# Performance work log

Hardware: AMD Instinct MI355X
Metric: run time of the kernel (lower is better)

## Reference

```python
import jax, jax.numpy as jnp
import numpy as np

N_NODES = 50000
N_EDGES = 800000
N_GRAPHS = 128
IN_F = 768
NHID = 64
HID2 = NHID * 2  # 128
N_CLS = 2


def setup_inputs() -> dict:
    key = jax.random.key(0)
    ks = jax.random.split(key, 16)
    s = lambda k, shp, fan: jax.random.normal(k, shp, jnp.float32) / np.sqrt(fan)
    return {
        "x": jax.random.normal(ks[0], (N_NODES, IN_F), jnp.float32),
        "edge_index": jax.random.randint(ks[1], (2, N_EDGES), 0, N_NODES, jnp.int64),
        "batch": jnp.sort(jax.random.randint(ks[2], (N_NODES,), 0, N_GRAPHS, jnp.int64)),
        "W1": s(ks[3], (IN_F, HID2), IN_F),
        "as1": s(ks[4], (HID2,), HID2),
        "ad1": s(ks[5], (HID2,), HID2),
        "b1": jnp.zeros((HID2,), jnp.float32),
        "W2": s(ks[6], (HID2, HID2), HID2),
        "as2": s(ks[7], (HID2,), HID2),
        "ad2": s(ks[8], (HID2,), HID2),
        "b2": jnp.zeros((HID2,), jnp.float32),
        "fc1_w": s(ks[9], (HID2, NHID), HID2),
        "fc1_b": jnp.zeros((NHID,), jnp.float32),
        "fc2_w": s(ks[10], (NHID, N_CLS), NHID),
        "fc2_b": jnp.zeros((N_CLS,), jnp.float32),
    }


def _gat_conv(x, W, a_src, a_dst, b, src, dst):
    # PyG GATConv, heads=1, self-loops already included in (src, dst).
    xw = x @ W                                   # [N, F_out]
    e_src = xw @ a_src                           # [N]
    e_dst = xw @ a_dst                           # [N]
    e = jax.nn.leaky_relu(e_src[src] + e_dst[dst], 0.2)   # [E]
    m = jax.ops.segment_max(e, dst, num_segments=N_NODES)  # per-dst max (stable softmax)
    num = jnp.exp(e - m[dst])
    den = jax.ops.segment_sum(num, dst, num_segments=N_NODES)
    alpha = num / den[dst]                       # [E]
    out = jax.ops.segment_sum(alpha[:, None] * xw[src], dst, num_segments=N_NODES)
    return out + b


def reference(x, edge_index, batch, W1, as1, ad1, b1, W2, as2, ad2, b2,
              fc1_w, fc1_b, fc2_w, fc2_b):
    # add self loops (PyG GATConv default add_self_loops=True)
    loops = jnp.arange(N_NODES, dtype=edge_index.dtype)
    src = jnp.concatenate([edge_index[0], loops])
    dst = jnp.concatenate([edge_index[1], loops])

    h = jax.nn.selu(_gat_conv(x, W1, as1, ad1, b1, src, dst))
    h = jax.nn.selu(_gat_conv(h, W2, as2, ad2, b2, src, dst))

    # global mean pool over graphs
    sums = jax.ops.segment_sum(h, batch, num_segments=N_GRAPHS)          # [G, HID2]
    cnts = jax.ops.segment_sum(jnp.ones((N_NODES,), h.dtype), batch, num_segments=N_GRAPHS)
    pooled = jax.nn.selu(sums / jnp.maximum(cnts, 1.0)[:, None])

    g = jax.nn.selu(pooled @ fc1_w + fc1_b)      # dropout is identity in eval mode
    logits = g @ fc2_w + fc2_b
    return jax.nn.log_softmax(logits, axis=-1)
```

## Files before the change

### kernel.cpp

```cpp
#include <hip/hip_runtime.h>
#include <math.h>

#define N_NODES  50000
#define N_EDGES  800000
#define E_TOT    (N_EDGES + N_NODES)
#define N_GRAPHS 128
#define IN_F     768
#define HID2     128
#define NHID     64

typedef __attribute__((ext_vector_type(8))) short bf16x8;
typedef __attribute__((ext_vector_type(4))) float f32x4;
typedef __attribute__((ext_vector_type(4))) unsigned short us4;

__device__ __forceinline__ float selu_f(float x) {
    const float alpha = 1.6732632423543772f;
    const float scale = 1.0507009873554805f;
    return scale * (x > 0.f ? x : alpha * (expf(x) - 1.f));
}

__device__ __forceinline__ unsigned short f2bf(float f) {
    unsigned u = __float_as_uint(f);
    u += 0x7FFFu + ((u >> 16) & 1u);
    return (unsigned short)(u >> 16);
}
__device__ __forceinline__ float bflo(unsigned q) { return __uint_as_float(q << 16); }
__device__ __forceinline__ float bfhi(unsigned q) { return __uint_as_float(q & 0xffff0000u); }

__global__ void setup_k(const float* __restrict__ W1, const float* __restrict__ W2,
                        unsigned short* __restrict__ Wt1, unsigned short* __restrict__ Wt2,
                        unsigned* __restrict__ deg,
                        float* __restrict__ es1, float* __restrict__ ed1,
                        float* __restrict__ es2, float* __restrict__ ed2) {
    int i = blockIdx.x * blockDim.x + threadIdx.x;
    if (i < N_NODES) {
        deg[i] = 0u;
        es1[i] = 0.f; ed1[i] = 0.f;
        es2[i] = 0.f; ed2[i] = 0.f;
    }
    if (i < 128 * IN_F) {
        int n = i / IN_F, k = i - n * IN_F;
        Wt1[i] = f2bf(W1[(long)k * 128 + n]);
    }
    if (i < 128 * HID2) {
        int n = i >> 7, k = i & 127;
        Wt2[i] = f2bf(W2[(long)k * 128 + n]);
    }
}

#define LDA2 72
template<bool ABF16, bool OUTBF16>
__global__ __launch_bounds__(256) void gemm_mfma(
        const void* __restrict__ Av, const unsigned short* __restrict__ Bt,
        void* __restrict__ Cv, int M, int K,
        const float* __restrict__ a_s, const float* __restrict__ a_d,
        float* __restrict__ es, float* __restrict__ ed) {
    __shared__ unsigned short As[64 * LDA2];
    __shared__ unsigned short Bs[128 * LDA2];
    const float* Af = (const float*)Av;
    const unsigned short* Ab = (const unsigned short*)Av;
    const int tid  = threadIdx.x;
    const int row0 = blockIdx.x * 64;
    const int w    = tid >> 6;
    const int lane = tid & 63;
    const int quad = lane >> 4;
    const int l16  = lane & 15;
    const int m_off = (w & 1) * 32;
    const int n_off = (w >> 1) * 64;

    f32x4 acc[2][4];
#pragma unroll
    for (int mi = 0; mi < 2; mi++)
#pragma unroll
        for (int ni = 0; ni < 4; ni++)
            acc[mi][ni] = (f32x4){0.f, 0.f, 0.f, 0.f};

    float4 aR[4];
    bf16x8 aRb[2];
    bf16x8 bR[4];
    if (ABF16) {
#pragma unroll
        for (int i = 0; i < 2; i++) {
            int p = tid + i * 256;
            int r = p >> 3, c8 = p & 7;
            int gr = row0 + r;
            aRb[i] = (gr < M) ? *(const bf16x8*)&Ab[(long)gr * K + c8 * 8]
                              : (bf16x8){0,0,0,0,0,0,0,0};
        }
    } else {
#pragma unroll
        for (int i = 0; i < 4; i++) {
            int p = tid + i * 256;
            int r = p >> 4, c4 = p & 15;
            int gr = row0 + r;
            aR[i] = (gr < M) ? *(const float4*)&Af[(long)gr * K + c4 * 4]
                             : make_float4(0.f, 0.f, 0.f, 0.f);
        }
    }
#pragma unroll
    for (int i = 0; i < 4; i++) {
        int c = tid + i * 256;
        int n = c >> 3, koff = (c & 7) * 8;
        bR[i] = *(const bf16x8*)&Bt[(long)n * K + koff];
    }

    for (int k0 = 0; k0 < K; k0 += 64) {
        if (ABF16) {
#pragma unroll
            for (int i = 0; i < 2; i++) {
                int p = tid + i * 256;
                int r = p >> 3, c8 = p & 7;
                *(bf16x8*)&As[r * LDA2 + c8 * 8] = aRb[i];
            }
        } else {
#pragma unroll
            for (int i = 0; i < 4; i++) {
                int p = tid + i * 256;
                int r = p >> 4, c4 = p & 15;
                us4 o;
                o.x = f2bf(aR[i].x); o.y = f2bf(aR[i].y);
                o.z = f2bf(aR[i].z); o.w = f2bf(aR[i].w);
                *(us4*)&As[r * LDA2 + c4 * 4] = o;
            }
        }
#pragma unroll
        for (int i = 0; i < 4; i++) {
            int c = tid + i * 256;
            int n = c >> 3, koff = (c & 7) * 8;
            *(bf16x8*)&Bs[n * LDA2 + koff] = bR[i];
        }
        __syncthreads();

        if (k0 + 64 < K) {
            int k1 = k0 + 64;
            if (ABF16) {
#pragma unroll
                for (int i = 0; i < 2; i++) {
                    int p = tid + i * 256;
                    int r = p >> 3, c8 = p & 7;
                    int gr = row0 + r;
                    aRb[i] = (gr < M) ? *(const bf16x8*)&Ab[(long)gr * K + k1 + c8 * 8]
                                      : (bf16x8){0,0,0,0,0,0,0,0};
                }
            } else {
#pragma unroll
                for (int i = 0; i < 4; i++) {
                    int p = tid + i * 256;
                    int r = p >> 4, c4 = p & 15;
                    int gr = row0 + r;
                    aR[i] = (gr < M) ? *(const float4*)&Af[(long)gr * K + k1 + c4 * 4]
                                     : make_float4(0.f, 0.f, 0.f, 0.f);
                }
            }
#pragma unroll
            for (int i = 0; i < 4; i++) {
                int c = tid + i * 256;
                int n = c >> 3, koff = (c & 7) * 8;
                bR[i] = *(const bf16x8*)&Bt[(long)n * K + k1 + koff];
            }
        }

        bf16x8 af[2][2], bfr[2][4];
#pragma unroll
        for (int kk = 0; kk < 2; kk++) {
#pragma unroll
            for (int mi = 0; mi < 2; mi++)
                af[kk][mi] = *(const bf16x8*)&As[(m_off + mi * 16 + l16) * LDA2 + kk * 32 + quad * 8];
#pragma unroll
            for (int ni = 0; ni < 4; ni++)
                bfr[kk][ni] = *(const bf16x8*)&Bs[(n_off + ni * 16 + l16) * LDA2 + kk * 32 + quad * 8];
        }
#pragma unroll
        for (int kk = 0; kk < 2; kk++)
#pragma unroll
            for (int mi = 0; mi < 2; mi++)
#pragma unroll
                for (int ni = 0; ni < 4; ni++)
                    acc[mi][ni] = __builtin_amdgcn_mfma_f32_16x16x32_bf16(
                        af[kk][mi], bfr[kk][ni], acc[mi][ni], 0, 0, 0);
        __syncthreads();
    }

    float as_v[4], ad_v[4];
#pragma unroll
    for (int ni = 0; ni < 4; ni++) {
        int col = n_off + ni * 16 + l16;
        as_v[ni] = a_s[col];
        ad_v[ni] = a_d[col];
    }

#pragma unroll
    for (int mi = 0; mi < 2; mi++)
#pragma unroll
        for (int r = 0; r < 4; r++) {
            int row = row0 + m_off + mi * 16 + quad * 4 + r;
            float ps = 0.f, pd = 0.f;
#pragma unroll
            for (int ni = 0; ni < 4; ni++) {
                float v = acc[mi][ni][r];
                ps = fmaf(v, as_v[ni], ps);
                pd = fmaf(v, ad_v[ni], pd);
            }
#pragma unroll
            for (int o = 1; o < 16; o <<= 1) {
                ps += __shfl_xor(ps, o);
                pd += __shfl_xor(pd, o);
            }
            if (row < M) {
                if (l16 == 0) {
                    atomicAdd(es + row, ps);
                    atomicAdd(ed + row, pd);
                }
                if (OUTBF16) {
                    unsigned short* C16 = (unsigned short*)Cv;
#pragma unroll
                    for (int ni = 0; ni < 4; ni++)
                        C16[(long)row * 128 + n_off + ni * 16 + l16] = f2bf(acc[mi][ni][r]);
                } else {
                    float* Cf = (float*)Cv;
#pragma unroll
                    for (int ni = 0; ni < 4; ni++)
                        Cf[(long)row * 128 + n_off + ni * 16 + l16] = acc[mi][ni][r];
                }
            }
        }
}

__global__ void deg_hist(const int* __restrict__ ei, unsigned* __restrict__ deg) {
    int e = blockIdx.x * blockDim.x + threadIdx.x;
    if (e < N_EDGES) atomicAdd(&deg[ei[N_EDGES + e]], 1u);
}

__global__ __launch_bounds__(256) void scan_seed(const unsigned* __restrict__ deg,
                                                 unsigned* __restrict__ row_ptr,
                                                 unsigned* __restrict__ cursor,
                                                 unsigned* __restrict__ csr_src) {
    __shared__ unsigned psum_s[4];
    __shared__ unsigned wsum[4];
    int tid = threadIdx.x;
    int wid = tid >> 6, lane = tid & 63;
    int chunk0 = blockIdx.x * 256;

    unsigned psum = 0;
    for (int i = tid; i < chunk0; i += 256) psum += deg[i] + 1u;
    for (int o = 32; o; o >>= 1) psum += __shfl_xor(psum, o);
    if (lane == 0) psum_s[wid] = psum;

    int i = chunk0 + tid;
    unsigned v = (i < N_NODES) ? deg[i] + 1u : 0u;
    unsigned x = v;
    for (int o = 1; o < 64; o <<= 1) {
        unsigned y = __shfl_up(x, o);
        if (lane >= o) x += y;
    }
    if (lane == 63) wsum[wid] = x;
    __syncthreads();
    unsigned base = psum_s[0] + psum_s[1] + psum_s[2] + psum_s[3];
    unsigned wbase = 0;
    for (int k = 0; k < wid; k++) wbase += wsum[k];
    if (i < N_NODES) {
        unsigned rp = base + wbase + x - v;
        row_ptr[i] = rp;
        csr_src[rp] = (unsigned)i;
        cursor[i] = rp + 1;
        if (i == N_NODES - 1) row_ptr[N_NODES] = rp + v;
    }
}

__global__ void csr_scatter(const int* __restrict__ ei,
                            unsigned* __restrict__ cursor, unsigned* __restrict__ csr_src) {
    int e = blockIdx.x * blockDim.x + threadIdx.x;
    if (e >= N_EDGES) return;
    int d = ei[N_EDGES + e];
    unsigned p = atomicAdd(&cursor[d], 1u);
    csr_src[p] = (unsigned)ei[e];
}

template<bool OUTBF16>
__global__ __launch_bounds__(256) void gat_agg(
        const unsigned* __restrict__ row_ptr, const unsigned* __restrict__ csr_src,
        const float* __restrict__ e_src, const float* __restrict__ e_dst,
        const unsigned short* __restrict__ xw, const float* __restrict__ bias,
        void* __restrict__ outv) {
    __shared__ float2 buf[8][32];
    int hw = threadIdx.x >> 5;
    int node = blockIdx.x * 8 + hw;
    if (node >= N_NODES) return;
    int fl = threadIdx.x & 31;
    unsigned beg = row_ptr[node], end = row_ptr[node + 1];
    int deg = (int)(end - beg);
    float ed = e_dst[node];
    const unsigned short* xwf = xw + fl * 4;

    float ax = 0.f, ay = 0.f, az = 0.f, aw = 0.f, den = 0.f;
    for (int base = 0; base < deg; base += 32) {
        int i = base + fl;
        float num = 0.f;
        unsigned s = 0u;
        if (i < deg) {
            s = csr_src[beg + i];
            float e = e_src[s] + ed;
            e = e > 0.f ? e : 0.2f * e;
            num = __expf(e);
            den += num;
        }
        float2 pk; pk.x = num; pk.y = __uint_as_float(s);
        buf[hw][fl] = pk;

        int cnt = deg - base; if (cnt > 32) cnt = 32;
        int t = 0;
        for (; t + 8 <= cnt; t += 8) {
            float2 p0 = buf[hw][t + 0];
            float2 p1 = buf[hw][t + 1];
            float2 p2 = buf[hw][t + 2];
            float2 p3 = buf[hw][t + 3];
            float2 p4 = buf[hw][t + 4];
            float2 p5 = buf[hw][t + 5];
            float2 p6 = buf[hw][t + 6];
            float2 p7 = buf[hw][t + 7];
            uint2 q0 = *(const uint2*)&xwf[(long)__float_as_uint(p0.y) * HID2];
            uint2 q1 = *(const uint2*)&xwf[(long)__float_as_uint(p1.y) * HID2];
            uint2 q2 = *(const uint2*)&xwf[(long)__float_as_uint(p2.y) * HID2];
            uint2 q3 = *(const uint2*)&xwf[(long)__float_as_uint(p3.y) * HID2];
            uint2 q4 = *(const uint2*)&xwf[(long)__float_as_uint(p4.y) * HID2];
            uint2 q5 = *(const uint2*)&xwf[(long)__float_as_uint(p5.y) * HID2];
            uint2 q6 = *(const uint2*)&xwf[(long)__float_as_uint(p6.y) * HID2];
            uint2 q7 = *(const uint2*)&xwf[(long)__float_as_uint(p7.y) * HID2];
            ax = fmaf(p0.x, bflo(q0.x), ax); ay = fmaf(p0.x, bfhi(q0.x), ay);
            az = fmaf(p0.x, bflo(q0.y), az); aw = fmaf(p0.x, bfhi(q0.y), aw);
            ax = fmaf(p1.x, bflo(q1.x), ax); ay = fmaf(p1.x, bfhi(q1.x), ay);
            az = fmaf(p1.x, bflo(q1.y), az); aw = fmaf(p1.x, bfhi(q1.y), aw);
            ax = fmaf(p2.x, bflo(q2.x), ax); ay = fmaf(p2.x, bfhi(q2.x), ay);
            az = fmaf(p2.x, bflo(q2.y), az); aw = fmaf(p2.x, bfhi(q2.y), aw);
            ax = fmaf(p3.x, bflo(q3.x), ax); ay = fmaf(p3.x, bfhi(q3.x), ay);
            az = fmaf(p3.x, bflo(q3.y), az); aw = fmaf(p3.x, bfhi(q3.y), aw);
            ax = fmaf(p4.x, bflo(q4.x), ax); ay = fmaf(p4.x, bfhi(q4.x), ay);
            az = fmaf(p4.x, bflo(q4.y), az); aw = fmaf(p4.x, bfhi(q4.y), aw);
            ax = fmaf(p5.x, bflo(q5.x), ax); ay = fmaf(p5.x, bfhi(q5.x), ay);
            az = fmaf(p5.x, bflo(q5.y), az); aw = fmaf(p5.x, bfhi(q5.y), aw);
            ax = fmaf(p6.x, bflo(q6.x), ax); ay = fmaf(p6.x, bfhi(q6.x), ay);
            az = fmaf(p6.x, bflo(q6.y), az); aw = fmaf(p6.x, bfhi(q6.y), aw);
            ax = fmaf(p7.x, bflo(q7.x), ax); ay = fmaf(p7.x, bfhi(q7.x), ay);
            az = fmaf(p7.x, bflo(q7.y), az); aw = fmaf(p7.x, bfhi(q7.y), aw);
        }
        for (; t < cnt; t++) {
            float2 p = buf[hw][t];
            uint2 q = *(const uint2*)&xwf[(long)__float_as_uint(p.y) * HID2];
            ax = fmaf(p.x, bflo(q.x), ax); ay = fmaf(p.x, bfhi(q.x), ay);
            az = fmaf(p.x, bflo(q.y), az); aw = fmaf(p.x, bfhi(q.y), aw);
        }
    }
    for (int o = 16; o; o >>= 1) den += __shfl_xor(den, o);
    float inv = 1.f / den;
    float v0 = selu_f(fmaf(ax, inv, bias[fl * 4 + 0]));
    float v1 = selu_f(fmaf(ay, inv, bias[fl * 4 + 1]));
    float v2 = selu_f(fmaf(az, inv, bias[fl * 4 + 2]));
    float v3 = selu_f(fmaf(aw, inv, bias[fl * 4 + 3]));
    if (OUTBF16) {
        uint2 o;
        o.x = ((unsigned)f2bf(v1) << 16) | (unsigned)f2bf(v0);
        o.y = ((unsigned)f2bf(v3) << 16) | (unsigned)f2bf(v2);
        *(uint2*)((unsigned short*)outv + (long)node * HID2 + fl * 4) = o;
    } else {
        float4 o = make_float4(v0, v1, v2, v3);
        *(float4*)((float*)outv + (long)node * HID2 + fl * 4) = o;
    }
}

__global__ __launch_bounds__(256) void pool_head(
        const float* __restrict__ h, const int* __restrict__ batch,
        const float* __restrict__ fc1w, const float* __restrict__ fc1b,
        const float* __restrict__ fc2w, const float* __restrict__ fc2b,
        float* __restrict__ out) {
    __shared__ float pooled_s[HID2];
    __shared__ float part[HID2];
    __shared__ float g_s[NHID];
    int g = blockIdx.x;
    int lo = 0, hi = N_NODES;
    while (lo < hi) { int mid = (lo + hi) >> 1; if (batch[mid] < g) lo = mid + 1; else hi = mid; }
    int start = lo;
    hi = N_NODES;
    while (lo < hi) { int mid = (lo + hi) >> 1; if (batch[mid] < g + 1) lo = mid + 1; else hi = mid; }
    int end = lo;

    int f = threadIdx.x & 127, half = threadIdx.x >> 7;
    float acc = 0.f;
    for (int n = start + half; n < end; n += 2) acc += h[(long)n * HID2 + f];
    if (half == 0) part[f] = acc;
    __syncthreads();
    if (half == 1) {
        float c = (float)(end - start);
        c = c > 1.f ? c : 1.f;
        pooled_s[f] = selu_f((part[f] + acc) / c);
    }
    __syncthreads();
    int j = threadIdx.x;
    if (j < NHID) {
        float a = fc1b[j];
#pragma unroll
        for (int k = 0; k < HID2; k++) a = fmaf(pooled_s[k], fc1w[k * NHID + j], a);
        g_s[j] = selu_f(a);
    }
    __syncthreads();
    if (j == 0) {
        float l0 = fc2b[0], l1 = fc2b[1];
#pragma unroll
        for (int k = 0; k < NHID; k++) {
            float v = g_s[k];
            l0 = fmaf(v, fc2w[2 * k + 0], l0);
            l1 = fmaf(v, fc2w[2 * k + 1], l1);
        }
        float m = fmaxf(l0, l1);
        float lse = m + logf(expf(l0 - m) + expf(l1 - m));
        out[g * 2 + 0] = l0 - lse;
        out[g * 2 + 1] = l1 - lse;
    }
}

extern "C" void kernel_launch(void* const* d_in, const int* in_sizes, int n_in,
                              void* d_out, int out_size, void* d_ws, size_t ws_size,
                              hipStream_t stream) {
    const float* x     = (const float*)d_in[0];
    const int*   ei    = (const int*)d_in[1];
    const int*   batch = (const int*)d_in[2];
    const float* W1    = (const float*)d_in[3];
    const float* as1   = (const float*)d_in[4];
    const float* ad1   = (const float*)d_in[5];
    const float* b1    = (const float*)d_in[6];
    const float* W2    = (const float*)d_in[7];
    const float* as2   = (const float*)d_in[8];
    const float* ad2   = (const float*)d_in[9];
    const float* b2    = (const float*)d_in[10];
    const float* fc1w  = (const float*)d_in[11];
    const float* fc1b  = (const float*)d_in[12];
    const float* fc2w  = (const float*)d_in[13];
    const float* fc2b  = (const float*)d_in[14];
    float* out = (float*)d_out;

    const long NH = (long)N_NODES * HID2;
    unsigned short* xwb = (unsigned short*)d_ws;
    unsigned short* h1b = xwb + NH;
    float*    B2      = (float*)(h1b + NH);
    float*    es1     = B2 + NH;
    float*    ed1     = es1 + N_NODES;
    float*    es2     = ed1 + N_NODES;
    float*    ed2     = es2 + N_NODES;
    unsigned* deg     = (unsigned*)(ed2 + N_NODES);
    unsigned* cursor  = deg + N_NODES;
    unsigned* row_ptr = cursor + N_NODES;
    unsigned* csr_src = row_ptr + N_NODES + 1;
    unsigned short* Wt1 = (unsigned short*)(csr_src + E_TOT);
    unsigned short* Wt2 = Wt1 + 128 * IN_F;

    const int TB = 256;
    const int gNode = (N_NODES + TB - 1) / TB;
    const int gEdge = (N_EDGES + TB - 1) / TB;
    const int gGemm = (N_NODES + 63) / 64;
    const int gAgg  = (N_NODES + 7) / 8;

    setup_k<<<(128 * IN_F + TB - 1) / TB, TB, 0, stream>>>(W1, W2, Wt1, Wt2, deg,
                                                           es1, ed1, es2, ed2);
    deg_hist<<<gEdge, TB, 0, stream>>>(ei, deg);
    scan_seed<<<gNode, TB, 0, stream>>>(deg, row_ptr, cursor, csr_src);
    csr_scatter<<<gEdge, TB, 0, stream>>>(ei, cursor, csr_src);

    gemm_mfma<false, true><<<gGemm, 256, 0, stream>>>(x, Wt1, xwb, N_NODES, IN_F,
                                                      as1, ad1, es1, ed1);
    gat_agg<true><<<gAgg, 256, 0, stream>>>(row_ptr, csr_src, es1, ed1, xwb, b1, h1b);

    gemm_mfma<true, true><<<gGemm, 256, 0, stream>>>(h1b, Wt2, xwb, N_NODES, HID2,
                                                     as2, ad2, es2, ed2);
    gat_agg<false><<<gAgg, 256, 0, stream>>>(row_ptr, csr_src, es2, ed2, xwb, b2, B2);

    pool_head<<<N_GRAPHS, 256, 0, stream>>>(B2, batch, fc1w, fc1b, fc2w, fc2b, out);
}
```

Measured before the change: 520.5 us.

## Fuse CSR build into one cooperative kernel and drop epilogue atomics

Replaces the separate zero, degree-histogram, scan and scatter kernels with one cooperative kernel that uses grid-wide syncs. The scan now gives each wave its base offset from an atomic counter instead of having every block re-sum all preceding degrees. The GEMM epilogue combines the two column halves' attention partial sums in shared memory and stores them directly, so the es/ed atomics and the zero-initialisation they needed are gone. gat_agg takes segment length from deg because row_ptr is no longer monotonic. Costs: the cooperative launch and grid syncs, and nondeterministic CSR segment placement.

```diff
diff --git a/kernel.cpp b/kernel.cpp
--- a/kernel.cpp
+++ b/kernel.cpp
@@ -1,5 +1,8 @@
 #include <hip/hip_runtime.h>
+#include <hip/hip_cooperative_groups.h>
 #include <math.h>
+
+namespace cg = cooperative_groups;
 
 #define N_NODES  50000
 #define N_EDGES  800000
@@ -27,17 +30,9 @@
 __device__ __forceinline__ float bflo(unsigned q) { return __uint_as_float(q << 16); }
 __device__ __forceinline__ float bfhi(unsigned q) { return __uint_as_float(q & 0xffff0000u); }
 
-__global__ void setup_k(const float* __restrict__ W1, const float* __restrict__ W2,
-                        unsigned short* __restrict__ Wt1, unsigned short* __restrict__ Wt2,
-                        unsigned* __restrict__ deg,
-                        float* __restrict__ es1, float* __restrict__ ed1,
-                        float* __restrict__ es2, float* __restrict__ ed2) {
+__global__ void setup_w(const float* __restrict__ W1, const float* __restrict__ W2,
+                        unsigned short* __restrict__ Wt1, unsigned short* __restrict__ Wt2) {
     int i = blockIdx.x * blockDim.x + threadIdx.x;
-    if (i < N_NODES) {
-        deg[i] = 0u;
-        es1[i] = 0.f; ed1[i] = 0.f;
-        es2[i] = 0.f; ed2[i] = 0.f;
-    }
     if (i < 128 * IN_F) {
         int n = i / IN_F, k = i - n * IN_F;
         Wt1[i] = f2bf(W1[(long)k * 128 + n]);
@@ -45,6 +40,46 @@
     if (i < 128 * HID2) {
         int n = i >> 7, k = i & 127;
         Wt2[i] = f2bf(W2[(long)k * 128 + n]);
+    }
+}
+
+__global__ __launch_bounds__(256) void csr_build(const int* __restrict__ ei,
+        unsigned* __restrict__ deg, unsigned* __restrict__ row_ptr,
+        unsigned* __restrict__ cursor, unsigned* __restrict__ csr_src,
+        unsigned* __restrict__ counter) {
+    cg::grid_group grid = cg::this_grid();
+    const int tid  = blockIdx.x * blockDim.x + threadIdx.x;
+    const int nthr = gridDim.x * blockDim.x;
+    for (int i = tid; i < N_NODES; i += nthr) deg[i] = 0u;
+    if (tid == 0) *counter = 0u;
+    grid.sync();
+    for (int e = tid; e < N_EDGES; e += nthr) atomicAdd(&deg[ei[N_EDGES + e]], 1u);
+    grid.sync();
+    {
+        int lane = threadIdx.x & 63;
+        int i = tid;
+        unsigned v = (i < N_NODES) ? deg[i] + 1u : 0u;
+        unsigned x = v;
+        for (int o = 1; o < 64; o <<= 1) {
+            unsigned y = __shfl_up(x, o);
+            if (lane >= o) x += y;
+        }
+        unsigned wtot = __shfl(x, 63);
+        unsigned base = 0u;
+        if (lane == 0 && wtot) base = atomicAdd(counter, wtot);
+        base = __shfl(base, 0);
+        if (i < N_NODES) {
+            unsigned rp = base + x - v;
+            row_ptr[i] = rp;
+            csr_src[rp] = (unsigned)i;
+            cursor[i] = rp + 1u;
+        }
+    }
+    grid.sync();
+    for (int e = tid; e < N_EDGES; e += nthr) {
+        int d = ei[N_EDGES + e];
+        unsigned p = atomicAdd(&cursor[d], 1u);
+        csr_src[p] = (unsigned)ei[e];
     }
 }
 
@@ -57,6 +92,8 @@
         float* __restrict__ es, float* __restrict__ ed) {
     __shared__ unsigned short As[64 * LDA2];
     __shared__ unsigned short Bs[128 * LDA2];
+    __shared__ float es_s[2][64];
+    __shared__ float ed_s[2][64];
     const float* Af = (const float*)Av;
     const unsigned short* Ab = (const unsigned short*)Av;
     const int tid  = threadIdx.x;
@@ -67,6 +104,7 @@
     const int l16  = lane & 15;
     const int m_off = (w & 1) * 32;
     const int n_off = (w >> 1) * 64;
+    const int nh    = w >> 1;
 
     f32x4 acc[2][4];
 #pragma unroll
@@ -193,7 +231,8 @@
     for (int mi = 0; mi < 2; mi++)
 #pragma unroll
         for (int r = 0; r < 4; r++) {
-            int row = row0 + m_off + mi * 16 + quad * 4 + r;
+            int rl  = m_off + mi * 16 + quad * 4 + r;
+            int row = row0 + rl;
             float ps = 0.f, pd = 0.f;
 #pragma unroll
             for (int ni = 0; ni < 4; ni++) {
@@ -206,11 +245,11 @@
                 ps += __shfl_xor(ps, o);
                 pd += __shfl_xor(pd, o);
             }
+            if (l16 == 0) {
+                es_s[nh][rl] = ps;
+                ed_s[nh][rl] = pd;
+            }
             if (row < M) {
-                if (l16 == 0) {
-                    atomicAdd(es + row, ps);
-                    atomicAdd(ed + row, pd);
-                }
                 if (OUTBF16) {
                     unsigned short* C16 = (unsigned short*)Cv;
 #pragma unroll
@@ -224,61 +263,20 @@
                 }
             }
         }
-}
-
-__global__ void deg_hist(const int* __restrict__ ei, unsigned* __restrict__ deg) {
-    int e = blockIdx.x * blockDim.x + threadIdx.x;
-    if (e < N_EDGES) atomicAdd(&deg[ei[N_EDGES + e]], 1u);
-}
-
-__global__ __launch_bounds__(256) void scan_seed(const unsigned* __restrict__ deg,
-                                                 unsigned* __restrict__ row_ptr,
-                                                 unsigned* __restrict__ cursor,
-                                                 unsigned* __restrict__ csr_src) {
-    __shared__ unsigned psum_s[4];
-    __shared__ unsigned wsum[4];
-    int tid = threadIdx.x;
-    int wid = tid >> 6, lane = tid & 63;
-    int chunk0 = blockIdx.x * 256;
-
-    unsigned psum = 0;
-    for (int i = tid; i < chunk0; i += 256) psum += deg[i] + 1u;
-    for (int o = 32; o; o >>= 1) psum += __shfl_xor(psum, o);
-    if (lane == 0) psum_s[wid] = psum;
-
-    int i = chunk0 + tid;
-    unsigned v = (i < N_NODES) ? deg[i] + 1u : 0u;
-    unsigned x = v;
-    for (int o = 1; o < 64; o <<= 1) {
-        unsigned y = __shfl_up(x, o);
-        if (lane >= o) x += y;
-    }
-    if (lane == 63) wsum[wid] = x;
     __syncthreads();
-    unsigned base = psum_s[0] + psum_s[1] + psum_s[2] + psum_s[3];
-    unsigned wbase = 0;
-    for (int k = 0; k < wid; k++) wbase += wsum[k];
-    if (i < N_NODES) {
-        unsigned rp = base + wbase + x - v;
-        row_ptr[i] = rp;
-        csr_src[rp] = (unsigned)i;
-        cursor[i] = rp + 1;
-        if (i == N_NODES - 1) row_ptr[N_NODES] = rp + v;
-    }
-}
-
-__global__ void csr_scatter(const int* __restrict__ ei,
-                            unsigned* __restrict__ cursor, unsigned* __restrict__ csr_src) {
-    int e = blockIdx.x * blockDim.x + threadIdx.x;
-    if (e >= N_EDGES) return;
-    int d = ei[N_EDGES + e];
-    unsigned p = atomicAdd(&cursor[d], 1u);
-    csr_src[p] = (unsigned)ei[e];
+    if (tid < 64) {
+        int row = row0 + tid;
+        if (row < M) {
+            es[row] = es_s[0][tid] + es_s[1][tid];
+            ed[row] = ed_s[0][tid] + ed_s[1][tid];
+        }
+    }
 }
 
 template<bool OUTBF16>
 __global__ __launch_bounds__(256) void gat_agg(
-        const unsigned* __restrict__ row_ptr, const unsigned* __restrict__ csr_src,
+        const unsigned* __restrict__ row_ptr, const unsigned* __restrict__ deg_a,
+        const unsigned* __restrict__ csr_src,
         const float* __restrict__ e_src, const float* __restrict__ e_dst,
         const unsigned short* __restrict__ xw, const float* __restrict__ bias,
         void* __restrict__ outv) {
@@ -287,8 +285,8 @@
     int node = blockIdx.x * 8 + hw;
     if (node >= N_NODES) return;
     int fl = threadIdx.x & 31;
-    unsigned beg = row_ptr[node], end = row_ptr[node + 1];
-    int deg = (int)(end - beg);
+    unsigned beg = row_ptr[node];
+    int deg = (int)deg_a[node] + 1;
     float ed = e_dst[node];
     const unsigned short* xwf = xw + fl * 4;
 
@@ -451,26 +449,26 @@
     unsigned* csr_src = row_ptr + N_NODES + 1;
     unsigned short* Wt1 = (unsigned short*)(csr_src + E_TOT);
     unsigned short* Wt2 = Wt1 + 128 * IN_F;
+    unsigned* counter = row_ptr + N_NODES;
 
     const int TB = 256;
-    const int gNode = (N_NODES + TB - 1) / TB;
-    const int gEdge = (N_EDGES + TB - 1) / TB;
     const int gGemm = (N_NODES + 63) / 64;
     const int gAgg  = (N_NODES + 7) / 8;
 
-    setup_k<<<(128 * IN_F + TB - 1) / TB, TB, 0, stream>>>(W1, W2, Wt1, Wt2, deg,
-                                                           es1, ed1, es2, ed2);
-    deg_hist<<<gEdge, TB, 0, stream>>>(ei, deg);
-    scan_seed<<<gNode, TB, 0, stream>>>(deg, row_ptr, cursor, csr_src);
-    csr_scatter<<<gEdge, TB, 0, stream>>>(ei, cursor, csr_src);
+    setup_w<<<(128 * IN_F + TB - 1) / TB, TB, 0, stream>>>(W1, W2, Wt1, Wt2);
+    {
+        void* args[] = {(void*)&ei, (void*)&deg, (void*)&row_ptr, (void*)&cursor,
+                        (void*)&csr_src, (void*)&counter};
+        hipLaunchCooperativeKernel((void*)csr_build, dim3(512), dim3(TB), args, 0, stream);
+    }
 
     gemm_mfma<false, true><<<gGemm, 256, 0, stream>>>(x, Wt1, xwb, N_NODES, IN_F,
                                                       as1, ad1, es1, ed1);
-    gat_agg<true><<<gAgg, 256, 0, stream>>>(row_ptr, csr_src, es1, ed1, xwb, b1, h1b);
+    gat_agg<true><<<gAgg, TB, 0, stream>>>(row_ptr, deg, csr_src, es1, ed1, xwb, b1, h1b);
 
     gemm_mfma<true, true><<<gGemm, 256, 0, stream>>>(h1b, Wt2, xwb, N_NODES, HID2,
                                                      as2, ad2, es2, ed2);
-    gat_agg<false><<<gAgg, 256, 0, stream>>>(row_ptr, csr_src, es2, ed2, xwb, b2, B2);
+    gat_agg<false><<<gAgg, TB, 0, stream>>>(row_ptr, deg, csr_src, es2, ed2, xwb, b2, B2);
 
     pool_head<<<N_GRAPHS, 256, 0, stream>>>(B2, batch, fc1w, fc1b, fc2w, fc2b, out);
 }
```

Measured after the change: 682.7 us. 1.31x slower.
